# Kernel tuning notes

Hardware: AMD Instinct MI355X
Metric: run time of the kernel (lower is better)

## Reference

```python
import jax, jax.numpy as jnp
import numpy as np

E, EDIM, NDIM, H = 262144, 256, 256, 8
DH = NDIM // H
EPS = 1e-5  # torch nn.LayerNorm default


def _param(k, shape, scale=0.02):
    return jax.random.normal(k, shape, jnp.float32) * scale


def setup_inputs() -> dict:
    key = jax.random.key(0)
    ks = jax.random.split(key, 12)
    return {
        "x": jax.random.normal(ks[0], (E, EDIM), jnp.float32),
        "src_x": jax.random.normal(ks[1], (E, NDIM), jnp.float32),
        "dst_x": jax.random.normal(ks[2], (E, NDIM), jnp.float32),
        # multi-head cross-attention params (q from edge feats, k/v from node feats)
        "Wq": _param(ks[3], (EDIM, NDIM)), "bq": jnp.zeros((NDIM,), jnp.float32),
        "Wk": _param(ks[4], (NDIM, NDIM)), "bk": jnp.zeros((NDIM,), jnp.float32),
        "Wv": _param(ks[5], (NDIM, NDIM)), "bv": jnp.zeros((NDIM,), jnp.float32),
        "Wo": _param(ks[6], (NDIM, EDIM)), "bo": jnp.zeros((EDIM,), jnp.float32),
        "W1": _param(ks[7], (EDIM, 4 * EDIM)), "b1": jnp.zeros((4 * EDIM,), jnp.float32),
        "W2": _param(ks[8], (4 * EDIM, EDIM)), "b2": jnp.zeros((EDIM,), jnp.float32),
        # two LayerNorms
        "g1": jnp.ones((EDIM,), jnp.float32), "be1": jnp.zeros((EDIM,), jnp.float32),
        "g2": jnp.ones((EDIM,), jnp.float32), "be2": jnp.zeros((EDIM,), jnp.float32),
    }


def _layer_norm(h, g, b):
    m = jnp.mean(h, axis=-1, keepdims=True)
    v = jnp.mean(jnp.square(h - m), axis=-1, keepdims=True)
    return (h - m) * jax.lax.rsqrt(v + EPS) * g + b


def reference(x, src_x, dst_x, Wq, bq, Wk, bk, Wv, bv, Wo, bo,
              W1, b1, W2, b2, g1, be1, g2, be2):
    # per-edge cross-attention: query = edge feat (len 1), keys/values = (src, dst) (len 2)
    q = (x @ Wq + bq).reshape(E, H, DH)                 # [E,H,DH]
    kv = jnp.stack([src_x, dst_x], axis=1)              # [E,2,NDIM]
    k = (kv @ Wk + bk).reshape(E, 2, H, DH)
    v = (kv @ Wv + bv).reshape(E, 2, H, DH)
    scale = 1.0 / float(np.sqrt(DH))
    scores = jnp.einsum('ehd,ekhd->ehk', q, k) * scale  # [E,H,2]
    attn = jax.nn.softmax(scores, axis=-1)
    ctx = jnp.einsum('ehk,ekhd->ehd', attn, v).reshape(E, NDIM)
    out = ctx @ Wo + bo                                  # [E,EDIM]
    h = _layer_norm(x + out, g1, be1)
    ff = jax.nn.relu(h @ W1 + b1) @ W2 + b2
    return _layer_norm(h + ff, g2, be2)
```

## Files before the change

kernel.cpp:

```cpp
#include <hip/hip_runtime.h>
#include <hip/hip_bf16.h>
#include <math.h>

#define NROWS   262144
#define BM      64
#define FBM     128
#define THREADS 256
#define FTHREADS 512
#define LDSB_A  (32768 + 32768 + 2048 + 512)
#define LDSB_B  (65536 + 65536)

using bf16x8 = __attribute__((ext_vector_type(8))) short;
using s16x4  = __attribute__((ext_vector_type(4))) short;
using f32x4  = __attribute__((ext_vector_type(4))) float;

__device__ __forceinline__ short f2bf(float f) {
  __hip_bfloat16 h = __float2bfloat16(f);
  return __builtin_bit_cast(short, h);
}
__device__ __forceinline__ float bf2f(short s) {
  __hip_bfloat16 h = __builtin_bit_cast(__hip_bfloat16, s);
  return __bfloat162float(h);
}
__device__ __forceinline__ unsigned pack2(float a, float b) {
  return (unsigned)(unsigned short)f2bf(a) | ((unsigned)(unsigned short)f2bf(b) << 16);
}
template <int RSTR>
__device__ __forceinline__ int swzR(int row, int col) {
  return row * RSTR + ((col * 2) ^ ((row & 7) << 4));
}
__device__ __forceinline__ int swz(int row, int col) {
  return swzR<512>(row, col);
}

__device__ __forceinline__ float red16(float p) {
  p += __shfl_xor(p, 1, 64);
  p += __shfl_xor(p, 2, 64);
  p += __shfl_xor(p, 4, 64);
  p += __shfl_xor(p, 8, 64);
  return p;
}

template <int MF, int NF, int KLEN = 256, int RSTR = 512>
__device__ __forceinline__ void gemmT(const char* __restrict__ Abuf,
                                      const short* __restrict__ WT, int Kw,
                                      int col0, int koff, int li, int hi,
                                      f32x4 (&acc)[MF][NF]) {
  const short* wp[NF];
#pragma unroll
  for (int n = 0; n < NF; ++n)
    wp[n] = WT + (size_t)(col0 + 16 * n + li) * Kw + koff + hi * 8;
#pragma unroll 2
  for (int kk = 0; kk < KLEN; kk += 32) {
    int ka = kk + hi * 8;
    bf16x8 b[NF];
#pragma unroll
    for (int n = 0; n < NF; ++n) b[n] = *(const bf16x8*)(wp[n] + kk);
    bf16x8 a[MF];
#pragma unroll
    for (int m = 0; m < MF; ++m)
      a[m] = *(const bf16x8*)(Abuf + swzR<RSTR>(16 * m + li, ka));
#pragma unroll
    for (int m = 0; m < MF; ++m)
#pragma unroll
      for (int n = 0; n < NF; ++n)
        acc[m][n] = __builtin_amdgcn_mfma_f32_16x16x32_bf16(a[m], b[n], acc[m][n], 0, 0, 0);
  }
}

__global__ void prep(const float* __restrict__ Wq, const float* __restrict__ Wk,
                     const float* __restrict__ Wv, const float* __restrict__ Wo,
                     const float* __restrict__ W1, const float* __restrict__ W2,
                     short* __restrict__ wt) {
  int idx = blockIdx.x * blockDim.x + threadIdx.x;
  if (idx < 262144) {
    int m = idx >> 16;
    const float* W = (m == 0) ? Wq : (m == 1) ? Wk : (m == 2) ? Wv : Wo;
    float s = (m == 0) ? 0.17677669529663687f : 1.0f;
    int l = idx & 65535;
    int n = l >> 8, k = l & 255;
    wt[idx] = f2bf(W[k * 256 + n] * s);
  } else if (idx < 524288) {
    int l = idx - 262144;
    int n = l >> 8, k = l & 255;
    wt[idx] = f2bf(W1[k * 1024 + n]);
  } else {
    int l = idx - 524288;
    int n = l >> 10, k = l & 1023;
    wt[idx] = f2bf(W2[k * 256 + n]);
  }
}

__global__ __launch_bounds__(THREADS, 2)
void attn_ln1(const float* __restrict__ x, const float* __restrict__ sx,
              const float* __restrict__ dx,
              const float* __restrict__ bq, const float* __restrict__ bv,
              const float* __restrict__ bo,
              const float* __restrict__ g1, const float* __restrict__ be1,
              const short* __restrict__ wt, short* __restrict__ hout) {
  extern __shared__ char sm[];
  char*  Cbuf = sm;
  char*  Tbuf = sm + 32768;
  float* sc   = (float*)(sm + 65536);
  float* scrM = (float*)(sm + 67584);

  const short* WqT = wt;
  const short* WkT = wt + 65536;
  const short* WvT = wt + 131072;
  const short* WoT = wt + 196608;

  const int tid  = threadIdx.x;
  const int w    = tid >> 6;
  const int lane = tid & 63;
  const int li   = lane & 15;
  const int hi   = lane >> 4;
  const int cw   = w * 64;
  const size_t row0 = (size_t)blockIdx.x * BM;

  const float* xt = x  + row0 * 256;
  const float* st = sx + row0 * 256;
  const float* dt = dx + row0 * 256;

  float4 ld[16];

#pragma unroll
  for (int it = 0; it < 16; ++it) {
    int idx = it * THREADS + tid;
    ld[it] = *(const float4*)(xt + (idx >> 6) * 256 + ((idx & 63) << 2));
  }
#pragma unroll
  for (int it = 0; it < 16; ++it) {
    int idx = it * THREADS + tid;
    int r = idx >> 6, c = (idx & 63) << 2;
    s16x4 o;
    o[0] = f2bf(ld[it].x); o[1] = f2bf(ld[it].y);
    o[2] = f2bf(ld[it].z); o[3] = f2bf(ld[it].w);
    *(s16x4*)(Cbuf + swz(r, c)) = o;
  }
  __syncthreads();

#pragma unroll
  for (int it = 0; it < 16; ++it) {
    int idx = it * THREADS + tid;
    ld[it] = *(const float4*)(dt + (idx >> 6) * 256 + ((idx & 63) << 2));
  }
  unsigned qb[4][4][2];
  {
    f32x4 qa[4][4];
#pragma unroll
    for (int m = 0; m < 4; ++m)
#pragma unroll
      for (int n = 0; n < 4; ++n) qa[m][n] = (f32x4){0.f, 0.f, 0.f, 0.f};
    gemmT<4, 4>(Cbuf, WqT, 256, cw, 0, li, hi, qa);
    const float scl = 0.17677669529663687f;
#pragma unroll
    for (int n = 0; n < 4; ++n) {
      float bqn = bq[cw + 16 * n + li] * scl;
#pragma unroll
      for (int m = 0; m < 4; ++m) {
        qb[m][n][0] = pack2(qa[m][n][0] + bqn, qa[m][n][1] + bqn);
        qb[m][n][1] = pack2(qa[m][n][2] + bqn, qa[m][n][3] + bqn);
      }
    }
  }
#pragma unroll
  for (int it = 0; it < 16; ++it) {
    int idx = it * THREADS + tid;
    int r = idx >> 6, c = (idx & 63) << 2;
    s16x4 o;
    o[0] = f2bf(ld[it].x); o[1] = f2bf(ld[it].y);
    o[2] = f2bf(ld[it].z); o[3] = f2bf(ld[it].w);
    *(s16x4*)(Tbuf + swz(r, c)) = o;
  }
  __syncthreads();

#define QF(m, n, j) bf2f((short)(((j) & 1) ? (qb[m][n][(j) >> 1] >> 16) \
                                           : (qb[m][n][(j) >> 1] & 0xffffu)))

#pragma unroll
  for (int it = 0; it < 16; ++it) {
    int idx = it * THREADS + tid;
    ld[it] = *(const float4*)(st + (idx >> 6) * 256 + ((idx & 63) << 2));
  }
#pragma unroll
  for (int hh = 0; hh < 2; ++hh) {
    f32x4 ka[4][2];
#pragma unroll
    for (int m = 0; m < 4; ++m)
#pragma unroll
      for (int n = 0; n < 2; ++n) ka[m][n] = (f32x4){0.f, 0.f, 0.f, 0.f};
    gemmT<4, 2>(Tbuf, WkT, 256, cw + 32 * hh, 0, li, hi, ka);
#pragma unroll
    for (int m = 0; m < 4; ++m)
#pragma unroll
      for (int j = 0; j < 4; ++j) {
        float pr = red16(QF(m, 2 * hh, j) * ka[m][0][j] +
                         QF(m, 2 * hh + 1, j) * ka[m][1][j]);
        if (li == 0) sc[(w * 2 + hh) * 64 + 16 * m + 4 * hi + j] = pr;
      }
  }
  f32x4 vd[4][4];
#pragma unroll
  for (int m = 0; m < 4; ++m)
#pragma unroll
    for (int n = 0; n < 4; ++n) vd[m][n] = (f32x4){0.f, 0.f, 0.f, 0.f};
  gemmT<4, 4>(Tbuf, WvT, 256, cw, 0, li, hi, vd);
  __syncthreads();
#pragma unroll
  for (int it = 0; it < 16; ++it) {
    int idx = it * THREADS + tid;
    int r = idx >> 6, c = (idx & 63) << 2;
    s16x4 o;
    o[0] = f2bf(ld[it].x); o[1] = f2bf(ld[it].y);
    o[2] = f2bf(ld[it].z); o[3] = f2bf(ld[it].w);
    *(s16x4*)(Tbuf + swz(r, c)) = o;
  }
  __syncthreads();

#pragma unroll
  for (int hh = 0; hh < 2; ++hh) {
    f32x4 ka[4][2];
#pragma unroll
    for (int m = 0; m < 4; ++m)
#pragma unroll
      for (int n = 0; n < 2; ++n) ka[m][n] = (f32x4){0.f, 0.f, 0.f, 0.f};
    gemmT<4, 2>(Tbuf, WkT, 256, cw + 32 * hh, 0, li, hi, ka);
#pragma unroll
    for (int m = 0; m < 4; ++m)
#pragma unroll
      for (int j = 0; j < 4; ++j) {
        float ps = red16(QF(m, 2 * hh, j) * ka[m][0][j] +
                         QF(m, 2 * hh + 1, j) * ka[m][1][j]);
        int r = 16 * m + 4 * hi + j;
        float pdv = sc[(w * 2 + hh) * 64 + r];
        float awv = 1.f / (1.f + expf(pdv - ps));
        if (li == 0) sc[(w * 2 + hh) * 64 + r] = awv;
      }
  }
  {
    f32x4 vs[4][4];
#pragma unroll
    for (int m = 0; m < 4; ++m)
#pragma unroll
      for (int n = 0; n < 4; ++n) vs[m][n] = (f32x4){0.f, 0.f, 0.f, 0.f};
    gemmT<4, 4>(Tbuf, WvT, 256, cw, 0, li, hi, vs);
#pragma unroll
    for (int hh = 0; hh < 2; ++hh)
#pragma unroll
      for (int n2 = 0; n2 < 2; ++n2) {
        int n = 2 * hh + n2;
        float bvn = bv[cw + 16 * n + li];
#pragma unroll
        for (int m = 0; m < 4; ++m)
#pragma unroll
          for (int j = 0; j < 4; ++j) {
            float a = sc[(w * 2 + hh) * 64 + 16 * m + 4 * hi + j];
            vs[m][n][j] = a * vs[m][n][j] + (1.f - a) * vd[m][n][j] + bvn;
          }
      }
    __syncthreads();
#pragma unroll
    for (int m = 0; m < 4; ++m)
#pragma unroll
      for (int n = 0; n < 4; ++n)
#pragma unroll
        for (int j = 0; j < 4; ++j)
          *(short*)(Tbuf + swz(16 * m + 4 * hi + j, cw + 16 * n + li)) = f2bf(vs[m][n][j]);
  }
  __syncthreads();

  {
    f32x4 oa[4][4];
#pragma unroll
    for (int m = 0; m < 4; ++m)
#pragma unroll
      for (int n = 0; n < 4; ++n) oa[m][n] = (f32x4){0.f, 0.f, 0.f, 0.f};
    gemmT<4, 4>(Tbuf, WoT, 256, cw, 0, li, hi, oa);
#pragma unroll
    for (int n = 0; n < 4; ++n) {
      float bon = bo[cw + 16 * n + li];
#pragma unroll
      for (int m = 0; m < 4; ++m)
#pragma unroll
        for (int j = 0; j < 4; ++j) {
          int r = 16 * m + 4 * hi + j;
          float xv = bf2f(*(short*)(Cbuf + swz(r, cw + 16 * n + li)));
          oa[m][n][j] += bon + xv;
        }
    }
#pragma unroll
    for (int m = 0; m < 4; ++m)
#pragma unroll
      for (int j = 0; j < 4; ++j) {
        int r = 16 * m + 4 * hi + j;
        float sv = oa[m][0][j] + oa[m][1][j] + oa[m][2][j] + oa[m][3][j];
        float qv = oa[m][0][j] * oa[m][0][j] + oa[m][1][j] * oa[m][1][j]
                 + oa[m][2][j] * oa[m][2][j] + oa[m][3][j] * oa[m][3][j];
        float s = red16(sv);
        float q = red16(qv);
        if (li == 0) { sc[(w * 64 + r) * 2] = s; sc[(w * 64 + r) * 2 + 1] = q; }
      }
    __syncthreads();
    if (tid < BM) {
      float S = 0.f, Q = 0.f;
#pragma unroll
      for (int ww = 0; ww < 4; ++ww) {
        S += sc[(ww * 64 + tid) * 2];
        Q += sc[(ww * 64 + tid) * 2 + 1];
      }
      float mean = S * (1.f / 256.f);
      float var  = Q * (1.f / 256.f) - mean * mean;
      scrM[tid * 2] = mean;
      scrM[tid * 2 + 1] = rsqrtf(var + 1e-5f);
    }
    __syncthreads();
#pragma unroll
    for (int n = 0; n < 4; ++n) {
      float g1n = g1[cw + 16 * n + li];
      float b1n = be1[cw + 16 * n + li];
#pragma unroll
      for (int m = 0; m < 4; ++m)
#pragma unroll
        for (int j = 0; j < 4; ++j) {
          int r = 16 * m + 4 * hi + j;
          float mean = scrM[r * 2], rs = scrM[r * 2 + 1];
          *(short*)(Cbuf + swz(r, cw + 16 * n + li)) =
              f2bf((oa[m][n][j] - mean) * rs * g1n + b1n);
        }
    }
  }
  __syncthreads();

  {
    short* hrow = hout + row0 * 256;
#pragma unroll
    for (int t = 0; t < 8; ++t) {
      int idx = t * THREADS + tid;
      int r = idx >> 5, c16 = idx & 31;
      bf16x8 v = *(bf16x8*)(Cbuf + r * 512 + ((c16 * 16) ^ ((r & 7) << 4)));
      *(bf16x8*)(hrow + r * 256 + c16 * 8) = v;
    }
  }
#undef QF
}

__global__ __launch_bounds__(FTHREADS, 2)
void ffn_ln2(const short* __restrict__ hin, const float* __restrict__ b1,
             const float* __restrict__ b2,
             const float* __restrict__ g2, const float* __restrict__ be2,
             const short* __restrict__ wt, float* __restrict__ out) {
  extern __shared__ char sm[];
  char* Cbuf = sm;
  char* Hbuf = sm + 65536;
  float* scrP = (float*)Hbuf;
  float* scrM = (float*)(Hbuf + 8192);

  const short* W1T = wt + 262144;
  const short* W2T = wt + 524288;

  const int tid  = threadIdx.x;
  const int w    = tid >> 6;
  const int lane = tid & 63;
  const int li   = lane & 15;
  const int hi   = lane >> 4;
  const int cw   = w * 32;
  const size_t row0 = (size_t)blockIdx.x * FBM;

  {
    const short* hrow = hin + row0 * 256;
#pragma unroll
    for (int t = 0; t < 8; ++t) {
      int idx = t * FTHREADS + tid;
      int r = idx >> 5, c16 = idx & 31;
      bf16x8 v = *(const bf16x8*)(hrow + r * 256 + c16 * 8);
      *(bf16x8*)(Cbuf + r * 512 + ((c16 * 16) ^ ((r & 7) << 4))) = v;
    }
  }
  __syncthreads();

  f32x4 a2[8][2];
#pragma unroll
  for (int m = 0; m < 8; ++m)
#pragma unroll
    for (int n = 0; n < 2; ++n) a2[m][n] = (f32x4){0.f, 0.f, 0.f, 0.f};
#pragma unroll 1
  for (int c = 0; c < 4; ++c) {
    f32x4 a1[8][2];
#pragma unroll
    for (int m = 0; m < 8; ++m)
#pragma unroll
      for (int n = 0; n < 2; ++n) a1[m][n] = (f32x4){0.f, 0.f, 0.f, 0.f};
    gemmT<8, 2, 256, 512>(Cbuf, W1T, 256, 256 * c + cw, 0, li, hi, a1);
#pragma unroll
    for (int n = 0; n < 2; ++n) {
      float b1n = b1[256 * c + cw + 16 * n + li];
      int lc = cw + 16 * n + li;
#pragma unroll
      for (int m = 0; m < 8; ++m)
#pragma unroll
        for (int j = 0; j < 4; ++j) {
          int r = 16 * m + 4 * hi + j;
          *(short*)(Hbuf + swzR<512>(r, lc)) = f2bf(fmaxf(a1[m][n][j] + b1n, 0.f));
        }
    }
    __syncthreads();
    gemmT<8, 2, 256, 512>(Hbuf, W2T, 1024, cw, 256 * c, li, hi, a2);
    __syncthreads();
  }

  {
#pragma unroll
    for (int n = 0; n < 2; ++n) {
      float b2n = b2[cw + 16 * n + li];
#pragma unroll
      for (int m = 0; m < 8; ++m)
#pragma unroll
        for (int j = 0; j < 4; ++j) {
          int r = 16 * m + 4 * hi + j;
          a2[m][n][j] += b2n + bf2f(*(short*)(Cbuf + swz(r, cw + 16 * n + li)));
        }
    }
  }
  __syncthreads();

#pragma unroll
  for (int m = 0; m < 8; ++m)
#pragma unroll
    for (int j = 0; j < 4; ++j) {
      int r = 16 * m + 4 * hi + j;
      float sv = a2[m][0][j] + a2[m][1][j];
      float qv = a2[m][0][j] * a2[m][0][j] + a2[m][1][j] * a2[m][1][j];
      float s = red16(sv);
      float q = red16(qv);
      if (li == 0) { scrP[(w * 128 + r) * 2] = s; scrP[(w * 128 + r) * 2 + 1] = q; }
    }
  __syncthreads();
  if (tid < FBM) {
    float S = 0.f, Q = 0.f;
#pragma unroll
    for (int ww = 0; ww < 8; ++ww) {
      S += scrP[(ww * 128 + tid) * 2];
      Q += scrP[(ww * 128 + tid) * 2 + 1];
    }
    float mean = S * (1.f / 256.f);
    float var  = Q * (1.f / 256.f) - mean * mean;
    scrM[tid * 2] = mean;
    scrM[tid * 2 + 1] = rsqrtf(var + 1e-5f);
  }
  __syncthreads();

  {
    float g2n[2], b2n[2];
#pragma unroll
    for (int n = 0; n < 2; ++n) {
      g2n[n] = g2[cw + 16 * n + li];
      b2n[n] = be2[cw + 16 * n + li];
    }
    float* orow = out + row0 * 256;
#pragma unroll
    for (int hf = 0; hf < 4; ++hf) {
#pragma unroll
      for (int m2 = 0; m2 < 2; ++m2) {
        int m = 2 * hf + m2;
#pragma unroll
        for (int n = 0; n < 2; ++n)
#pragma unroll
          for (int j = 0; j < 4; ++j) {
            int r = 16 * m + 4 * hi + j;
            float mean = scrM[r * 2], rs = scrM[r * 2 + 1];
            int rr = r - 32 * hf;
            *(float*)(Cbuf + rr * 1024 + (((cw + 16 * n + li) * 4) ^ ((rr & 7) << 4)))
                = (a2[m][n][j] - mean) * rs * g2n[n] + b2n[n];
          }
      }
      __syncthreads();
#pragma unroll
      for (int t = 0; t < 4; ++t) {
        int idx = t * FTHREADS + tid;
        int r = idx >> 6, c4 = idx & 63;
        f32x4 v = *(f32x4*)(Cbuf + r * 1024 + ((c4 * 16) ^ ((r & 7) << 4)));
        *(f32x4*)(orow + (hf * 32 + r) * 256 + c4 * 4) = v;
      }
      __syncthreads();
    }
  }
}

extern "C" void kernel_launch(void* const* d_in, const int* in_sizes, int n_in,
                              void* d_out, int out_size, void* d_ws, size_t ws_size,
                              hipStream_t stream) {
  const float* x   = (const float*)d_in[0];
  const float* sx  = (const float*)d_in[1];
  const float* dx  = (const float*)d_in[2];
  const float* Wq  = (const float*)d_in[3];
  const float* bq  = (const float*)d_in[4];
  const float* Wk  = (const float*)d_in[5];
  const float* Wv  = (const float*)d_in[7];
  const float* bv  = (const float*)d_in[8];
  const float* Wo  = (const float*)d_in[9];
  const float* bo  = (const float*)d_in[10];
  const float* W1  = (const float*)d_in[11];
  const float* b1  = (const float*)d_in[12];
  const float* W2  = (const float*)d_in[13];
  const float* b2  = (const float*)d_in[14];
  const float* g1  = (const float*)d_in[15];
  const float* be1 = (const float*)d_in[16];
  const float* g2  = (const float*)d_in[17];
  const float* be2 = (const float*)d_in[18];
  short* wt = (short*)d_ws;
  short* hbuf = wt + 786432;

  prep<<<dim3(1536), dim3(512), 0, stream>>>(Wq, Wk, Wv, Wo, W1, W2, wt);
  attn_ln1<<<dim3(NROWS / BM), dim3(THREADS), LDSB_A, stream>>>(
      x, sx, dx, bq, bv, bo, g1, be1, wt, hbuf);
  ffn_ln2<<<dim3(NROWS / FBM), dim3(FTHREADS), LDSB_B, stream>>>(
      hbuf, b1, b2, g2, be2, wt, (float*)d_out);
}
```

Before: 1.090 ms.

## Retile attention kernel to 128-row blocks with 8 waves of 32 columns

The attention+LN1 kernel now processes 128 rows per block with 512 threads. Each of the 8 waves owns a 32-column slice (one head) across all 128 rows, instead of 64 rows by 64 columns. This doubles the row reuse of each weight fragment loaded from global memory and halves the number of blocks. In exchange it needs much more LDS per block (about 145KB), which likely limits occupancy to one block per CU, and the LN partial sums now go to a separate scratch area.

```diff
diff --git a/kernel.cpp b/kernel.cpp
--- a/kernel.cpp
+++ b/kernel.cpp
@@ -3,11 +3,11 @@
 #include <math.h>
 
 #define NROWS   262144
-#define BM      64
+#define ABM     128
 #define FBM     128
-#define THREADS 256
+#define ATHREADS 512
 #define FTHREADS 512
-#define LDSB_A  (32768 + 32768 + 2048 + 512)
+#define LDSB_A  (65536 + 65536 + 4096 + 8192 + 1024)
 #define LDSB_B  (65536 + 65536)
 
 using bf16x8 = __attribute__((ext_vector_type(8))) short;
@@ -91,7 +91,7 @@
   }
 }
 
-__global__ __launch_bounds__(THREADS, 2)
+__global__ __launch_bounds__(ATHREADS, 2)
 void attn_ln1(const float* __restrict__ x, const float* __restrict__ sx,
               const float* __restrict__ dx,
               const float* __restrict__ bq, const float* __restrict__ bv,
@@ -100,9 +100,10 @@
               const short* __restrict__ wt, short* __restrict__ hout) {
   extern __shared__ char sm[];
   char*  Cbuf = sm;
-  char*  Tbuf = sm + 32768;
-  float* sc   = (float*)(sm + 65536);
-  float* scrM = (float*)(sm + 67584);
+  char*  Tbuf = sm + 65536;
+  float* sc   = (float*)(sm + 131072);
+  float* scrP = (float*)(sm + 135168);
+  float* scrM = (float*)(sm + 143360);
 
   const short* WqT = wt;
   const short* WkT = wt + 65536;
@@ -114,8 +115,8 @@
   const int lane = tid & 63;
   const int li   = lane & 15;
   const int hi   = lane >> 4;
-  const int cw   = w * 64;
-  const size_t row0 = (size_t)blockIdx.x * BM;
+  const int cw   = w * 32;
+  const size_t row0 = (size_t)blockIdx.x * ABM;
 
   const float* xt = x  + row0 * 256;
   const float* st = sx + row0 * 256;
@@ -125,12 +126,12 @@
 
 #pragma unroll
   for (int it = 0; it < 16; ++it) {
-    int idx = it * THREADS + tid;
+    int idx = it * ATHREADS + tid;
     ld[it] = *(const float4*)(xt + (idx >> 6) * 256 + ((idx & 63) << 2));
   }
 #pragma unroll
   for (int it = 0; it < 16; ++it) {
-    int idx = it * THREADS + tid;
+    int idx = it * ATHREADS + tid;
     int r = idx >> 6, c = (idx & 63) << 2;
     s16x4 o;
     o[0] = f2bf(ld[it].x); o[1] = f2bf(ld[it].y);
@@ -141,23 +142,23 @@
 
 #pragma unroll
   for (int it = 0; it < 16; ++it) {
-    int idx = it * THREADS + tid;
+    int idx = it * ATHREADS + tid;
     ld[it] = *(const float4*)(dt + (idx >> 6) * 256 + ((idx & 63) << 2));
   }
-  unsigned qb[4][4][2];
-  {
-    f32x4 qa[4][4];
-#pragma unroll
-    for (int m = 0; m < 4; ++m)
-#pragma unroll
-      for (int n = 0; n < 4; ++n) qa[m][n] = (f32x4){0.f, 0.f, 0.f, 0.f};
-    gemmT<4, 4>(Cbuf, WqT, 256, cw, 0, li, hi, qa);
+  unsigned qb[8][2][2];
+  {
+    f32x4 qa[8][2];
+#pragma unroll
+    for (int m = 0; m < 8; ++m)
+#pragma unroll
+      for (int n = 0; n < 2; ++n) qa[m][n] = (f32x4){0.f, 0.f, 0.f, 0.f};
+    gemmT<8, 2>(Cbuf, WqT, 256, cw, 0, li, hi, qa);
     const float scl = 0.17677669529663687f;
 #pragma unroll
-    for (int n = 0; n < 4; ++n) {
+    for (int n = 0; n < 2; ++n) {
       float bqn = bq[cw + 16 * n + li] * scl;
 #pragma unroll
-      for (int m = 0; m < 4; ++m) {
+      for (int m = 0; m < 8; ++m) {
         qb[m][n][0] = pack2(qa[m][n][0] + bqn, qa[m][n][1] + bqn);
         qb[m][n][1] = pack2(qa[m][n][2] + bqn, qa[m][n][3] + bqn);
       }
@@ -165,7 +166,7 @@
   }
 #pragma unroll
   for (int it = 0; it < 16; ++it) {
-    int idx = it * THREADS + tid;
+    int idx = it * ATHREADS + tid;
     int r = idx >> 6, c = (idx & 63) << 2;
     s16x4 o;
     o[0] = f2bf(ld[it].x); o[1] = f2bf(ld[it].y);
@@ -179,36 +180,34 @@
 
 #pragma unroll
   for (int it = 0; it < 16; ++it) {
-    int idx = it * THREADS + tid;
+    int idx = it * ATHREADS + tid;
     ld[it] = *(const float4*)(st + (idx >> 6) * 256 + ((idx & 63) << 2));
   }
-#pragma unroll
-  for (int hh = 0; hh < 2; ++hh) {
-    f32x4 ka[4][2];
-#pragma unroll
-    for (int m = 0; m < 4; ++m)
+  {
+    f32x4 ka[8][2];
+#pragma unroll
+    for (int m = 0; m < 8; ++m)
 #pragma unroll
       for (int n = 0; n < 2; ++n) ka[m][n] = (f32x4){0.f, 0.f, 0.f, 0.f};
-    gemmT<4, 2>(Tbuf, WkT, 256, cw + 32 * hh, 0, li, hi, ka);
-#pragma unroll
-    for (int m = 0; m < 4; ++m)
+    gemmT<8, 2>(Tbuf, WkT, 256, cw, 0, li, hi, ka);
+#pragma unroll
+    for (int m = 0; m < 8; ++m)
 #pragma unroll
       for (int j = 0; j < 4; ++j) {
-        float pr = red16(QF(m, 2 * hh, j) * ka[m][0][j] +
-                         QF(m, 2 * hh + 1, j) * ka[m][1][j]);
-        if (li == 0) sc[(w * 2 + hh) * 64 + 16 * m + 4 * hi + j] = pr;
-      }
-  }
-  f32x4 vd[4][4];
-#pragma unroll
-  for (int m = 0; m < 4; ++m)
-#pragma unroll
-    for (int n = 0; n < 4; ++n) vd[m][n] = (f32x4){0.f, 0.f, 0.f, 0.f};
-  gemmT<4, 4>(Tbuf, WvT, 256, cw, 0, li, hi, vd);
+        float pr = red16(QF(m, 0, j) * ka[m][0][j] + QF(m, 1, j) * ka[m][1][j]);
+        if (li == 0) sc[w * 128 + 16 * m + 4 * hi + j] = pr;
+      }
+  }
+  f32x4 vd[8][2];
+#pragma unroll
+  for (int m = 0; m < 8; ++m)
+#pragma unroll
+    for (int n = 0; n < 2; ++n) vd[m][n] = (f32x4){0.f, 0.f, 0.f, 0.f};
+  gemmT<8, 2>(Tbuf, WvT, 256, cw, 0, li, hi, vd);
   __syncthreads();
 #pragma unroll
   for (int it = 0; it < 16; ++it) {
-    int idx = it * THREADS + tid;
+    int idx = it * ATHREADS + tid;
     int r = idx >> 6, c = (idx & 63) << 2;
     s16x4 o;
     o[0] = f2bf(ld[it].x); o[1] = f2bf(ld[it].y);
@@ -217,52 +216,47 @@
   }
   __syncthreads();
 
-#pragma unroll
-  for (int hh = 0; hh < 2; ++hh) {
-    f32x4 ka[4][2];
-#pragma unroll
-    for (int m = 0; m < 4; ++m)
+  {
+    f32x4 ka[8][2];
+#pragma unroll
+    for (int m = 0; m < 8; ++m)
 #pragma unroll
       for (int n = 0; n < 2; ++n) ka[m][n] = (f32x4){0.f, 0.f, 0.f, 0.f};
-    gemmT<4, 2>(Tbuf, WkT, 256, cw + 32 * hh, 0, li, hi, ka);
-#pragma unroll
-    for (int m = 0; m < 4; ++m)
+    gemmT<8, 2>(Tbuf, WkT, 256, cw, 0, li, hi, ka);
+#pragma unroll
+    for (int m = 0; m < 8; ++m)
 #pragma unroll
       for (int j = 0; j < 4; ++j) {
-        float ps = red16(QF(m, 2 * hh, j) * ka[m][0][j] +
-                         QF(m, 2 * hh + 1, j) * ka[m][1][j]);
+        float ps = red16(QF(m, 0, j) * ka[m][0][j] + QF(m, 1, j) * ka[m][1][j]);
         int r = 16 * m + 4 * hi + j;
-        float pdv = sc[(w * 2 + hh) * 64 + r];
+        float pdv = sc[w * 128 + r];
         float awv = 1.f / (1.f + expf(pdv - ps));
-        if (li == 0) sc[(w * 2 + hh) * 64 + r] = awv;
-      }
-  }
-  {
-    f32x4 vs[4][4];
-#pragma unroll
-    for (int m = 0; m < 4; ++m)
-#pragma unroll
-      for (int n = 0; n < 4; ++n) vs[m][n] = (f32x4){0.f, 0.f, 0.f, 0.f};
-    gemmT<4, 4>(Tbuf, WvT, 256, cw, 0, li, hi, vs);
-#pragma unroll
-    for (int hh = 0; hh < 2; ++hh)
-#pragma unroll
-      for (int n2 = 0; n2 < 2; ++n2) {
-        int n = 2 * hh + n2;
-        float bvn = bv[cw + 16 * n + li];
-#pragma unroll
-        for (int m = 0; m < 4; ++m)
-#pragma unroll
-          for (int j = 0; j < 4; ++j) {
-            float a = sc[(w * 2 + hh) * 64 + 16 * m + 4 * hi + j];
-            vs[m][n][j] = a * vs[m][n][j] + (1.f - a) * vd[m][n][j] + bvn;
-          }
-      }
+        if (li == 0) sc[w * 128 + r] = awv;
+      }
+  }
+  {
+    f32x4 vs[8][2];
+#pragma unroll
+    for (int m = 0; m < 8; ++m)
+#pragma unroll
+      for (int n = 0; n < 2; ++n) vs[m][n] = (f32x4){0.f, 0.f, 0.f, 0.f};
+    gemmT<8, 2>(Tbuf, WvT, 256, cw, 0, li, hi, vs);
+#pragma unroll
+    for (int n = 0; n < 2; ++n) {
+      float bvn = bv[cw + 16 * n + li];
+#pragma unroll
+      for (int m = 0; m < 8; ++m)
+#pragma unroll
+        for (int j = 0; j < 4; ++j) {
+          float a = sc[w * 128 + 16 * m + 4 * hi + j];
+          vs[m][n][j] = a * vs[m][n][j] + (1.f - a) * vd[m][n][j] + bvn;
+        }
+    }
     __syncthreads();
 #pragma unroll
-    for (int m = 0; m < 4; ++m)
-#pragma unroll
-      for (int n = 0; n < 4; ++n)
+    for (int m = 0; m < 8; ++m)
+#pragma unroll
+      for (int n = 0; n < 2; ++n)
 #pragma unroll
         for (int j = 0; j < 4; ++j)
           *(short*)(Tbuf + swz(16 * m + 4 * hi + j, cw + 16 * n + li)) = f2bf(vs[m][n][j]);
@@ -270,17 +264,17 @@
   __syncthreads();
 
   {
-    f32x4 oa[4][4];
-#pragma unroll
-    for (int m = 0; m < 4; ++m)
-#pragma unroll
-      for (int n = 0; n < 4; ++n) oa[m][n] = (f32x4){0.f, 0.f, 0.f, 0.f};
-    gemmT<4, 4>(Tbuf, WoT, 256, cw, 0, li, hi, oa);
-#pragma unroll
-    for (int n = 0; n < 4; ++n) {
+    f32x4 oa[8][2];
+#pragma unroll
+    for (int m = 0; m < 8; ++m)
+#pragma unroll
+      for (int n = 0; n < 2; ++n) oa[m][n] = (f32x4){0.f, 0.f, 0.f, 0.f};
+    gemmT<8, 2>(Tbuf, WoT, 256, cw, 0, li, hi, oa);
+#pragma unroll
+    for (int n = 0; n < 2; ++n) {
       float bon = bo[cw + 16 * n + li];
 #pragma unroll
-      for (int m = 0; m < 4; ++m)
+      for (int m = 0; m < 8; ++m)
 #pragma unroll
         for (int j = 0; j < 4; ++j) {
           int r = 16 * m + 4 * hi + j;
@@ -289,24 +283,23 @@
         }
     }
 #pragma unroll
-    for (int m = 0; m < 4; ++m)
+    for (int m = 0; m < 8; ++m)
 #pragma unroll
       for (int j = 0; j < 4; ++j) {
         int r = 16 * m + 4 * hi + j;
-        float sv = oa[m][0][j] + oa[m][1][j] + oa[m][2][j] + oa[m][3][j];
-        float qv = oa[m][0][j] * oa[m][0][j] + oa[m][1][j] * oa[m][1][j]
-                 + oa[m][2][j] * oa[m][2][j] + oa[m][3][j] * oa[m][3][j];
+        float sv = oa[m][0][j] + oa[m][1][j];
+        float qv = oa[m][0][j] * oa[m][0][j] + oa[m][1][j] * oa[m][1][j];
         float s = red16(sv);
         float q = red16(qv);
-        if (li == 0) { sc[(w * 64 + r) * 2] = s; sc[(w * 64 + r) * 2 + 1] = q; }
+        if (li == 0) { scrP[(w * 128 + r) * 2] = s; scrP[(w * 128 + r) * 2 + 1] = q; }
       }
     __syncthreads();
-    if (tid < BM) {
+    if (tid < ABM) {
       float S = 0.f, Q = 0.f;
 #pragma unroll
-      for (int ww = 0; ww < 4; ++ww) {
-        S += sc[(ww * 64 + tid) * 2];
-        Q += sc[(ww * 64 + tid) * 2 + 1];
+      for (int ww = 0; ww < 8; ++ww) {
+        S += scrP[(ww * 128 + tid) * 2];
+        Q += scrP[(ww * 128 + tid) * 2 + 1];
       }
       float mean = S * (1.f / 256.f);
       float var  = Q * (1.f / 256.f) - mean * mean;
@@ -315,11 +308,11 @@
     }
     __syncthreads();
 #pragma unroll
-    for (int n = 0; n < 4; ++n) {
+    for (int n = 0; n < 2; ++n) {
       float g1n = g1[cw + 16 * n + li];
       float b1n = be1[cw + 16 * n + li];
 #pragma unroll
-      for (int m = 0; m < 4; ++m)
+      for (int m = 0; m < 8; ++m)
 #pragma unroll
         for (int j = 0; j < 4; ++j) {
           int r = 16 * m + 4 * hi + j;
@@ -335,7 +328,7 @@
     short* hrow = hout + row0 * 256;
 #pragma unroll
     for (int t = 0; t < 8; ++t) {
-      int idx = t * THREADS + tid;
+      int idx = t * ATHREADS + tid;
       int r = idx >> 5, c16 = idx & 31;
       bf16x8 v = *(bf16x8*)(Cbuf + r * 512 + ((c16 * 16) ^ ((r & 7) << 4)));
       *(bf16x8*)(hrow + r * 256 + c16 * 8) = v;
@@ -511,7 +504,7 @@
   short* hbuf = wt + 786432;
 
   prep<<<dim3(1536), dim3(512), 0, stream>>>(Wq, Wk, Wv, Wo, W1, W2, wt);
-  attn_ln1<<<dim3(NROWS / BM), dim3(THREADS), LDSB_A, stream>>>(
+  attn_ln1<<<dim3(NROWS / ABM), dim3(ATHREADS), LDSB_A, stream>>>(
       x, sx, dx, bq, bv, bo, g1, be1, wt, hbuf);
   ffn_ln2<<<dim3(NROWS / FBM), dim3(FTHREADS), LDSB_B, stream>>>(
       hbuf, b1, b2, g2, be2, wt, (float*)d_out);
```

Measured after the change: 1.096 ms. Within noise of the previous version (+0.6%).
